# Kernel tuning notes

Measured on AMD Instinct MI355X. Metric: run time of the kernel, lower is better.

## Reference

```python
import jax, jax.numpy as jnp
import numpy as np

QMAX = 127.0  # 2**(8-1) - 1 for n_bits=8

def fake_quant_last_dim(t):
    # per-row absmax fake quant over last dim (per-token for acts, per-channel for weights)
    scales = jnp.max(jnp.abs(t), axis=-1, keepdims=True)
    scales = jnp.clip(scales, 1e-05, None) / QMAX
    return jnp.round(t / scales) * scales

def setup_inputs() -> dict:
    key = jax.random.key(0)
    k1, k2, k3 = jax.random.split(key, 3)
    B, S, D_in, D_out = 4, 2048, 4096, 4096
    return {
        "input": jax.random.normal(k1, (B, S, D_in), dtype=jnp.float32),
        "weight": jax.random.normal(k2, (D_out, D_in), dtype=jnp.float32) * 0.02,
        "bias": jax.random.normal(k3, (D_out,), dtype=jnp.float32) * 0.02,
    }

def reference(input, weight, bias):
    w_q = fake_quant_last_dim(weight)          # per-output-channel
    x_q = fake_quant_last_dim(input)           # per-token
    y = jnp.einsum('bsi,oi->bso', x_q, w_q) + bias
    return fake_quant_last_dim(y)              # per-token output quant
```

## Files before the change

### kernel.cpp

```cpp
#include <hip/hip_runtime.h>

typedef unsigned int u32;
typedef __attribute__((ext_vector_type(4))) int i32x4;

#define BM 256
#define BN 256
#define BKT 128

__device__ __forceinline__ void gload16(const void* g, void* l) {
  __builtin_amdgcn_global_load_lds(
      (const __attribute__((address_space(1))) unsigned int*)g,
      (__attribute__((address_space(3))) unsigned int*)l, 16, 0, 0);
}

__device__ __forceinline__ u32 pack4_i8(float4 v, float scale) {
  const int a = (int)rintf(v.x / scale);
  const int b = (int)rintf(v.y / scale);
  const int c = (int)rintf(v.z / scale);
  const int d = (int)rintf(v.w / scale);
  return (u32)(a & 255) | (((u32)(b & 255)) << 8) |
         (((u32)(c & 255)) << 16) | (((u32)(d & 255)) << 24);
}

__global__ __launch_bounds__(256) void quant_rows4096_kernel(
    const float* __restrict__ src, u32* __restrict__ q,
    float* __restrict__ scales)
{
  const size_t row = blockIdx.x;
  const float4* __restrict__ p = (const float4*)(src + row * 4096);
  const int t = threadIdx.x;
  float4 v0 = p[t];
  float4 v1 = p[t + 256];
  float4 v2 = p[t + 512];
  float4 v3 = p[t + 768];
  float m = 0.0f;
  m = fmaxf(m, fmaxf(fmaxf(fabsf(v0.x), fabsf(v0.y)), fmaxf(fabsf(v0.z), fabsf(v0.w))));
  m = fmaxf(m, fmaxf(fmaxf(fabsf(v1.x), fabsf(v1.y)), fmaxf(fabsf(v1.z), fabsf(v1.w))));
  m = fmaxf(m, fmaxf(fmaxf(fabsf(v2.x), fabsf(v2.y)), fmaxf(fabsf(v2.z), fabsf(v2.w))));
  m = fmaxf(m, fmaxf(fmaxf(fabsf(v3.x), fabsf(v3.y)), fmaxf(fabsf(v3.z), fabsf(v3.w))));
  #pragma unroll
  for (int off = 32; off > 0; off >>= 1) m = fmaxf(m, __shfl_xor(m, off));
  __shared__ float wmax[4];
  if ((t & 63) == 0) wmax[t >> 6] = m;
  __syncthreads();
  m = fmaxf(fmaxf(wmax[0], wmax[1]), fmaxf(wmax[2], wmax[3]));
  const float scale = fmaxf(m, 1e-5f) * (1.0f / 127.0f);
  if (t == 0) scales[row] = scale;
  u32* __restrict__ qp = q + row * 1024;
  qp[t]       = pack4_i8(v0, scale);
  qp[t + 256] = pack4_i8(v1, scale);
  qp[t + 512] = pack4_i8(v2, scale);
  qp[t + 768] = pack4_i8(v3, scale);
}

__global__ __launch_bounds__(256) void quant_rows_kernel(
    const float* __restrict__ src, u32* __restrict__ q,
    float* __restrict__ scales, int K)
{
  const size_t row = blockIdx.x;
  const float* __restrict__ p = src + row * (size_t)K;
  const int t = threadIdx.x;
  const int nv = K >> 2;
  float m = 0.0f;
  for (int i = t; i < nv; i += 256) {
    float4 v = ((const float4*)p)[i];
    m = fmaxf(m, fmaxf(fmaxf(fabsf(v.x), fabsf(v.y)),
                       fmaxf(fabsf(v.z), fabsf(v.w))));
  }
  #pragma unroll
  for (int off = 32; off > 0; off >>= 1) m = fmaxf(m, __shfl_xor(m, off));
  __shared__ float wmax[4];
  if ((t & 63) == 0) wmax[t >> 6] = m;
  __syncthreads();
  m = fmaxf(fmaxf(wmax[0], wmax[1]), fmaxf(wmax[2], wmax[3]));
  const float scale = fmaxf(m, 1e-5f) * (1.0f / 127.0f);
  if (t == 0) scales[row] = scale;
  u32* __restrict__ qp = q + row * ((size_t)K >> 2);
  for (int i = t; i < nv; i += 256) {
    float4 v = ((const float4*)p)[i];
    qp[i] = pack4_i8(v, scale);
  }
}

__global__ __launch_bounds__(512, 2) void gemm_bt_kernel(
    const signed char* __restrict__ Aq, const signed char* __restrict__ Bq,
    const float* __restrict__ sx, const float* __restrict__ sw,
    const float* __restrict__ bias, float* __restrict__ Y,
    unsigned int* __restrict__ rowmax, int M, int N, int K)
{
  __shared__ signed char lds[2][2][BM * 128];

  int bid = (int)blockIdx.x;
  const int nwg = (int)gridDim.x;
  if ((nwg & 7) == 0) {
    const int cpx = nwg >> 3;
    bid = (bid & 7) * cpx + (bid >> 3);
  }
  const int ntile = N / BN;
  const size_t brow = (size_t)(bid / ntile) * BM;
  const size_t bcol = (size_t)(bid % ntile) * BN;

  const int t = threadIdx.x;
  const int lane = t & 63;
  const int wid = t >> 6;
  const int wr = wid >> 2, wc = wid & 3;
  const int g4 = lane >> 4, l16 = lane & 15, l7 = lane & 7;

  const int aRow = wr * 128 + l16;
  const int bRow = wc * 64 + l16;
  const int col0 = ((g4) ^ l7) * 16;
  const int col1 = ((4 + g4) ^ l7) * 16;

  const int tr = t >> 3, ts = t & 7;
  const int sslot = ts ^ (tr & 7);
  const signed char* srcA = Aq + (brow + tr) * (size_t)K + sslot * 16;
  const signed char* srcB = Bq + (bcol + tr) * (size_t)K + sslot * 16;
  const int dst = t * 16;

  i32x4 acc0[4][4] = {};
  i32x4 acc1[4][4] = {};
  const int nK = K / BKT;

  i32x4 aA0, aA1, aA2, aA3;
  i32x4 aB0, aB1, aB2, aB3;
  i32x4 aC0, aC1, aC2, aC3;
  i32x4 aD0, aD1, aD2, aD3;
  i32x4 bA0, bA1, bA2, bA3;
  i32x4 bB0, bB1, bB2, bB3;

#define STA(S, R, TT) gload16(srcA + ((size_t)(R) * 64) * (size_t)K + (size_t)(TT) * BKT, \
                              &lds[S][0][(R) * 8192 + dst])
#define STB(S, R, TT) gload16(srcB + ((size_t)(R) * 64) * (size_t)K + (size_t)(TT) * BKT, \
                              &lds[S][1][(R) * 8192 + dst])
#define BARS() do { asm volatile("" ::: "memory"); \
                    __builtin_amdgcn_s_barrier(); \
                    asm volatile("" ::: "memory"); } while (0)
#define VMWS(NN) asm volatile("s_waitcnt vmcnt(" #NN ")" ::: "memory")
#define RDA(P, S, MH, COL) do { \
    P##0 = *(const i32x4*)&lds[S][0][(aRow + (MH) * 64 +  0) * 128 + (COL)]; \
    P##1 = *(const i32x4*)&lds[S][0][(aRow + (MH) * 64 + 16) * 128 + (COL)]; \
    P##2 = *(const i32x4*)&lds[S][0][(aRow + (MH) * 64 + 32) * 128 + (COL)]; \
    P##3 = *(const i32x4*)&lds[S][0][(aRow + (MH) * 64 + 48) * 128 + (COL)]; } while (0)
#define RDB(P, S, COL) do { \
    P##0 = *(const i32x4*)&lds[S][1][(bRow +  0) * 128 + (COL)]; \
    P##1 = *(const i32x4*)&lds[S][1][(bRow + 16) * 128 + (COL)]; \
    P##2 = *(const i32x4*)&lds[S][1][(bRow + 32) * 128 + (COL)]; \
    P##3 = *(const i32x4*)&lds[S][1][(bRow + 48) * 128 + (COL)]; } while (0)
#define MF(ACC, A, B) do { \
    __builtin_amdgcn_s_setprio(1); \
    ACC[0][0] = __builtin_amdgcn_mfma_i32_16x16x64_i8(A##0, B##0, ACC[0][0], 0, 0, 0); \
    ACC[0][1] = __builtin_amdgcn_mfma_i32_16x16x64_i8(A##0, B##1, ACC[0][1], 0, 0, 0); \
    ACC[0][2] = __builtin_amdgcn_mfma_i32_16x16x64_i8(A##0, B##2, ACC[0][2], 0, 0, 0); \
    ACC[0][3] = __builtin_amdgcn_mfma_i32_16x16x64_i8(A##0, B##3, ACC[0][3], 0, 0, 0); \
    ACC[1][0] = __builtin_amdgcn_mfma_i32_16x16x64_i8(A##1, B##0, ACC[1][0], 0, 0, 0); \
    ACC[1][1] = __builtin_amdgcn_mfma_i32_16x16x64_i8(A##1, B##1, ACC[1][1], 0, 0, 0); \
    ACC[1][2] = __builtin_amdgcn_mfma_i32_16x16x64_i8(A##1, B##2, ACC[1][2], 0, 0, 0); \
    ACC[1][3] = __builtin_amdgcn_mfma_i32_16x16x64_i8(A##1, B##3, ACC[1][3], 0, 0, 0); \
    ACC[2][0] = __builtin_amdgcn_mfma_i32_16x16x64_i8(A##2, B##0, ACC[2][0], 0, 0, 0); \
    ACC[2][1] = __builtin_amdgcn_mfma_i32_16x16x64_i8(A##2, B##1, ACC[2][1], 0, 0, 0); \
    ACC[2][2] = __builtin_amdgcn_mfma_i32_16x16x64_i8(A##2, B##2, ACC[2][2], 0, 0, 0); \
    ACC[2][3] = __builtin_amdgcn_mfma_i32_16x16x64_i8(A##2, B##3, ACC[2][3], 0, 0, 0); \
    ACC[3][0] = __builtin_amdgcn_mfma_i32_16x16x64_i8(A##3, B##0, ACC[3][0], 0, 0, 0); \
    ACC[3][1] = __builtin_amdgcn_mfma_i32_16x16x64_i8(A##3, B##1, ACC[3][1], 0, 0, 0); \
    ACC[3][2] = __builtin_amdgcn_mfma_i32_16x16x64_i8(A##3, B##2, ACC[3][2], 0, 0, 0); \
    ACC[3][3] = __builtin_amdgcn_mfma_i32_16x16x64_i8(A##3, B##3, ACC[3][3], 0, 0, 0); \
    __builtin_amdgcn_s_setprio(0); } while (0)

#define BODY(S, SN, TS) do { \
     \
    RDA(aA, S, 0, col0); RDB(bA, S, col0); \
    STA(SN, 0, TS); STA(SN, 2, TS); STB(SN, 0, TS); STB(SN, 1, TS); \
    BARS(); MF(acc0, aA, bA); BARS(); \
     \
    RDA(aB, S, 0, col1); RDB(bB, S, col1); \
    STB(SN, 2, TS); STB(SN, 3, TS); STA(SN, 1, TS); STA(SN, 3, TS); \
    VMWS(8); \
    BARS(); MF(acc0, aB, bB); BARS(); \
     \
    RDA(aC, S, 1, col0); \
    BARS(); MF(acc1, aC, bA); BARS(); \
     \
    RDA(aD, S, 1, col1); \
    VMWS(2); \
    BARS(); MF(acc1, aD, bB); BARS(); \
  } while (0)

  STA(0, 0, 0); STA(0, 2, 0); STB(0, 0, 0); STB(0, 1, 0);
  STB(0, 2, 0); STB(0, 3, 0); STA(0, 1, 0); STA(0, 3, 0);
  VMWS(2);
  BARS();

  for (int kt = 0; kt < nK - 2; kt += 2) {
    BODY(0, 1, kt + 1);
    BODY(1, 0, kt + 2);
  }
  BODY(0, 1, nK - 1);

  {
    RDA(aA, 1, 0, col0); RDB(bA, 1, col0);
    BARS(); MF(acc0, aA, bA); BARS();
    RDA(aB, 1, 0, col1); RDB(bB, 1, col1);
    VMWS(0);
    BARS(); MF(acc0, aB, bB); BARS();
    RDA(aC, 1, 1, col0);
    BARS(); MF(acc1, aC, bA); BARS();
    RDA(aD, 1, 1, col1);
    BARS(); MF(acc1, aD, bB);
  }

  float swv[4], biv[4];
  size_t gcolv[4];
  #pragma unroll
  for (int j = 0; j < 4; ++j) {
    gcolv[j] = bcol + wc * 64 + j * 16 + l16;
    swv[j] = sw[gcolv[j]];
    biv[j] = bias[gcolv[j]];
  }
  #pragma unroll
  for (int mh = 0; mh < 2; ++mh) {
    #pragma unroll
    for (int i = 0; i < 4; ++i) {
      #pragma unroll
      for (int r = 0; r < 4; ++r) {
        const size_t grow = brow + (size_t)(wr * 128 + mh * 64 + i * 16 + g4 * 4 + r);
        const float sxr = sx[grow];
        float* yrow = Y + grow * (size_t)N;
        float rmax = 0.0f;
        #pragma unroll
        for (int j = 0; j < 4; ++j) {
          const int av = mh ? acc1[i][j][r] : acc0[i][j][r];
          const float y = (float)av * (sxr * swv[j]) + biv[j];
          yrow[gcolv[j]] = y;
          rmax = fmaxf(rmax, fabsf(y));
        }
        rmax = fmaxf(rmax, __shfl_xor(rmax, 1));
        rmax = fmaxf(rmax, __shfl_xor(rmax, 2));
        rmax = fmaxf(rmax, __shfl_xor(rmax, 4));
        rmax = fmaxf(rmax, __shfl_xor(rmax, 8));
        if (l16 == 0)
          atomicMax(&rowmax[grow], __float_as_uint(rmax));
      }
    }
  }
#undef STA
#undef STB
#undef BARS
#undef VMWS
#undef RDA
#undef RDB
#undef MF
#undef BODY
}

__global__ __launch_bounds__(256) void outquant_kernel(
    float* __restrict__ Y, const unsigned int* __restrict__ rowmax, int N)
{
  const size_t row = blockIdx.x;
  const float amax = __uint_as_float(rowmax[row]);
  const float scale = fmaxf(amax, 1e-5f) * (1.0f / 127.0f);
  float* __restrict__ p = Y + row * (size_t)N;
  const int nv = N >> 2;
  for (int i = threadIdx.x; i < nv; i += 256) {
    float4 v = ((float4*)p)[i];
    v.x = rintf(v.x / scale) * scale;
    v.y = rintf(v.y / scale) * scale;
    v.z = rintf(v.z / scale) * scale;
    v.w = rintf(v.w / scale) * scale;
    ((float4*)p)[i] = v;
  }
}

extern "C" void kernel_launch(void* const* d_in, const int* in_sizes, int n_in,
                              void* d_out, int out_size, void* d_ws, size_t ws_size,
                              hipStream_t stream)
{
  const float* x = (const float*)d_in[0];
  const float* wgt = (const float*)d_in[1];
  const float* bias = (const float*)d_in[2];
  float* out = (float*)d_out;

  const int N = in_sizes[2];
  const int K = in_sizes[1] / N;
  const int M = in_sizes[0] / K;

  char* ws = (char*)d_ws;
  signed char* qx = (signed char*)ws;  ws += (size_t)M * K;
  signed char* qw = (signed char*)ws;  ws += (size_t)N * K;
  float* sx = (float*)ws;              ws += (size_t)M * sizeof(float);
  float* sw = (float*)ws;              ws += (size_t)N * sizeof(float);
  unsigned int* rowmax = (unsigned int*)ws;

  hipMemsetAsync(rowmax, 0, (size_t)M * sizeof(unsigned int), stream);

  if (K == 4096) {
    quant_rows4096_kernel<<<M, 256, 0, stream>>>(x, (u32*)qx, sx);
    quant_rows4096_kernel<<<N, 256, 0, stream>>>(wgt, (u32*)qw, sw);
  } else {
    quant_rows_kernel<<<M, 256, 0, stream>>>(x, (u32*)qx, sx, K);
    quant_rows_kernel<<<N, 256, 0, stream>>>(wgt, (u32*)qw, sw, K);
  }

  const int grid = (M / BM) * (N / BN);
  gemm_bt_kernel<<<grid, 512, 0, stream>>>(qx, qw, sx, sw, bias, out, rowmax, M, N, K);

  outquant_kernel<<<M, 256, 0, stream>>>(out, rowmax, N);
}
```

Before: 250.5 us.

## Load B operand directly from global into registers, bypassing LDS

The weight (B) tile is no longer staged through shared memory. Each wave now loads its B fragments straight from global memory into registers, double-buffered across K steps, and LDS holds only the A tile, which halves shared-memory use. This removes LDS writes and reads for B. In exchange, B is fetched redundantly by the two wave rows with uncoalesced per-lane 16-byte loads, register pressure rises with 16 extra i32x4 values, and the wait moves to vmcnt(0) each iteration, which may stall.

```diff
diff --git a/kernel.cpp b/kernel.cpp
--- a/kernel.cpp
+++ b/kernel.cpp
@@ -88,7 +88,7 @@
     const float* __restrict__ bias, float* __restrict__ Y,
     unsigned int* __restrict__ rowmax, int M, int N, int K)
 {
-  __shared__ signed char lds[2][2][BM * 128];
+  __shared__ signed char lds[2][BM * 128];
 
   int bid = (int)blockIdx.x;
   const int nwg = (int)gridDim.x;
@@ -107,15 +107,16 @@
   const int g4 = lane >> 4, l16 = lane & 15, l7 = lane & 7;
 
   const int aRow = wr * 128 + l16;
-  const int bRow = wc * 64 + l16;
   const int col0 = ((g4) ^ l7) * 16;
   const int col1 = ((4 + g4) ^ l7) * 16;
 
   const int tr = t >> 3, ts = t & 7;
   const int sslot = ts ^ (tr & 7);
   const signed char* srcA = Aq + (brow + tr) * (size_t)K + sslot * 16;
-  const signed char* srcB = Bq + (bcol + tr) * (size_t)K + sslot * 16;
   const int dst = t * 16;
+
+  const int kq = K >> 4;
+  const i32x4* __restrict__ Bg = (const i32x4*)Bq + (bcol + wc * 64 + l16) * (size_t)kq;
 
   i32x4 acc0[4][4] = {};
   i32x4 acc1[4][4] = {};
@@ -125,27 +126,30 @@
   i32x4 aB0, aB1, aB2, aB3;
   i32x4 aC0, aC1, aC2, aC3;
   i32x4 aD0, aD1, aD2, aD3;
-  i32x4 bA0, bA1, bA2, bA3;
-  i32x4 bB0, bB1, bB2, bB3;
+  i32x4 bEA0, bEA1, bEA2, bEA3, bEB0, bEB1, bEB2, bEB3;
+  i32x4 bOA0, bOA1, bOA2, bOA3, bOB0, bOB1, bOB2, bOB3;
 
 #define STA(S, R, TT) gload16(srcA + ((size_t)(R) * 64) * (size_t)K + (size_t)(TT) * BKT, \
-                              &lds[S][0][(R) * 8192 + dst])
-#define STB(S, R, TT) gload16(srcB + ((size_t)(R) * 64) * (size_t)K + (size_t)(TT) * BKT, \
-                              &lds[S][1][(R) * 8192 + dst])
+                              &lds[S][(R) * 8192 + dst])
+#define STAGEA(S, TT) do { STA(S, 0, TT); STA(S, 1, TT); STA(S, 2, TT); STA(S, 3, TT); } while (0)
 #define BARS() do { asm volatile("" ::: "memory"); \
                     __builtin_amdgcn_s_barrier(); \
                     asm volatile("" ::: "memory"); } while (0)
 #define VMWS(NN) asm volatile("s_waitcnt vmcnt(" #NN ")" ::: "memory")
 #define RDA(P, S, MH, COL) do { \
-    P##0 = *(const i32x4*)&lds[S][0][(aRow + (MH) * 64 +  0) * 128 + (COL)]; \
-    P##1 = *(const i32x4*)&lds[S][0][(aRow + (MH) * 64 + 16) * 128 + (COL)]; \
-    P##2 = *(const i32x4*)&lds[S][0][(aRow + (MH) * 64 + 32) * 128 + (COL)]; \
-    P##3 = *(const i32x4*)&lds[S][0][(aRow + (MH) * 64 + 48) * 128 + (COL)]; } while (0)
-#define RDB(P, S, COL) do { \
-    P##0 = *(const i32x4*)&lds[S][1][(bRow +  0) * 128 + (COL)]; \
-    P##1 = *(const i32x4*)&lds[S][1][(bRow + 16) * 128 + (COL)]; \
-    P##2 = *(const i32x4*)&lds[S][1][(bRow + 32) * 128 + (COL)]; \
-    P##3 = *(const i32x4*)&lds[S][1][(bRow + 48) * 128 + (COL)]; } while (0)
+    P##0 = *(const i32x4*)&lds[S][(aRow + (MH) * 64 +  0) * 128 + (COL)]; \
+    P##1 = *(const i32x4*)&lds[S][(aRow + (MH) * 64 + 16) * 128 + (COL)]; \
+    P##2 = *(const i32x4*)&lds[S][(aRow + (MH) * 64 + 32) * 128 + (COL)]; \
+    P##3 = *(const i32x4*)&lds[S][(aRow + (MH) * 64 + 48) * 128 + (COL)]; } while (0)
+#define LOADB(PA, PB, TT) do { \
+    PA##0 = Bg[ 0 * kq + (TT) * 8 +     g4]; \
+    PA##1 = Bg[16 * kq + (TT) * 8 +     g4]; \
+    PA##2 = Bg[32 * kq + (TT) * 8 +     g4]; \
+    PA##3 = Bg[48 * kq + (TT) * 8 +     g4]; \
+    PB##0 = Bg[ 0 * kq + (TT) * 8 + 4 + g4]; \
+    PB##1 = Bg[16 * kq + (TT) * 8 + 4 + g4]; \
+    PB##2 = Bg[32 * kq + (TT) * 8 + 4 + g4]; \
+    PB##3 = Bg[48 * kq + (TT) * 8 + 4 + g4]; } while (0)
 #define MF(ACC, A, B) do { \
     __builtin_amdgcn_s_setprio(1); \
     ACC[0][0] = __builtin_amdgcn_mfma_i32_16x16x64_i8(A##0, B##0, ACC[0][0], 0, 0, 0); \
@@ -166,46 +170,44 @@
     ACC[3][3] = __builtin_amdgcn_mfma_i32_16x16x64_i8(A##3, B##3, ACC[3][3], 0, 0, 0); \
     __builtin_amdgcn_s_setprio(0); } while (0)
 
-#define BODY(S, SN, TS) do { \
+#define BODY(S, SN, TT, BCA, BCB, BNA, BNB) do { \
      \
-    RDA(aA, S, 0, col0); RDB(bA, S, col0); \
-    STA(SN, 0, TS); STA(SN, 2, TS); STB(SN, 0, TS); STB(SN, 1, TS); \
-    BARS(); MF(acc0, aA, bA); BARS(); \
+    RDA(aA, S, 0, col0); \
+    STAGEA(SN, TT); \
+    BARS(); MF(acc0, aA, BCA); BARS(); \
      \
-    RDA(aB, S, 0, col1); RDB(bB, S, col1); \
-    STB(SN, 2, TS); STB(SN, 3, TS); STA(SN, 1, TS); STA(SN, 3, TS); \
-    VMWS(8); \
-    BARS(); MF(acc0, aB, bB); BARS(); \
+    RDA(aB, S, 0, col1); \
+    LOADB(BNA, BNB, TT); \
+    BARS(); MF(acc0, aB, BCB); BARS(); \
      \
     RDA(aC, S, 1, col0); \
-    BARS(); MF(acc1, aC, bA); BARS(); \
+    BARS(); MF(acc1, aC, BCA); BARS(); \
      \
     RDA(aD, S, 1, col1); \
-    VMWS(2); \
-    BARS(); MF(acc1, aD, bB); BARS(); \
+    VMWS(0); \
+    BARS(); MF(acc1, aD, BCB); BARS(); \
   } while (0)
 
-  STA(0, 0, 0); STA(0, 2, 0); STB(0, 0, 0); STB(0, 1, 0);
-  STB(0, 2, 0); STB(0, 3, 0); STA(0, 1, 0); STA(0, 3, 0);
-  VMWS(2);
+  STAGEA(0, 0);
+  LOADB(bEA, bEB, 0);
+  VMWS(0);
   BARS();
 
   for (int kt = 0; kt < nK - 2; kt += 2) {
-    BODY(0, 1, kt + 1);
-    BODY(1, 0, kt + 2);
-  }
-  BODY(0, 1, nK - 1);
+    BODY(0, 1, kt + 1, bEA, bEB, bOA, bOB);
+    BODY(1, 0, kt + 2, bOA, bOB, bEA, bEB);
+  }
+  BODY(0, 1, nK - 1, bEA, bEB, bOA, bOB);
 
   {
-    RDA(aA, 1, 0, col0); RDB(bA, 1, col0);
-    BARS(); MF(acc0, aA, bA); BARS();
-    RDA(aB, 1, 0, col1); RDB(bB, 1, col1);
-    VMWS(0);
-    BARS(); MF(acc0, aB, bB); BARS();
+    RDA(aA, 1, 0, col0);
+    BARS(); MF(acc0, aA, bOA); BARS();
+    RDA(aB, 1, 0, col1);
+    BARS(); MF(acc0, aB, bOB); BARS();
     RDA(aC, 1, 1, col0);
-    BARS(); MF(acc1, aC, bA); BARS();
+    BARS(); MF(acc1, aC, bOA); BARS();
     RDA(aD, 1, 1, col1);
-    BARS(); MF(acc1, aD, bB);
+    BARS(); MF(acc1, aD, bOB);
   }
 
   float swv[4], biv[4];
@@ -243,11 +245,11 @@
     }
   }
 #undef STA
-#undef STB
+#undef STAGEA
 #undef BARS
 #undef VMWS
 #undef RDA
-#undef RDB
+#undef LOADB
 #undef MF
 #undef BODY
 }
```

After: 346.3 us. 1.38x slower.
